# Performance work log

Hardware: AMD Instinct MI355X
Metric: run time of the kernel (lower is better)

The kernel has to match this reference:

```python
import jax, jax.numpy as jnp
import numpy as np

B, S, IN, OUT, RANK, NLANG = 4, 4096, 1024, 4096, 32, 9


def setup_inputs() -> dict:
    key = jax.random.key(0)
    k_x, k_w, k_w1 = jax.random.split(key, 3)
    x = jax.random.normal(k_x, (B, S, IN), dtype=jnp.float32)
    # base Linear weight (xavier-uniform in torch; gaussian fine for a numeric baseline)
    weight = jax.random.normal(k_w, (OUT, IN), dtype=jnp.float32) * 0.02
    bias = jnp.zeros((OUT,), dtype=jnp.float32)
    # per-language low-rank factors; torch inits w1 ~ N(0, 0.01), w2 zeros --
    # use small random values for both so gradients/outputs are non-trivial
    w1 = jax.random.normal(k_w1, (NLANG, OUT, RANK), dtype=jnp.float32) * 0.01
    w2 = jax.random.normal(jax.random.fold_in(key, 7), (NLANG, RANK, IN), dtype=jnp.float32) * 0.01
    return {"x": x, "weight": weight, "bias": bias, "w1": w1, "w2": w2,
            "src_id": 0, "tgt_id": 3}


def reference(x, weight, bias, w1, w2, src_id, tgt_id):
    # pair LMS delta: full [OUT, IN] low-rank matrix, as in the torch module
    delta = w1[src_id] @ w2[tgt_id]          # [OUT, RANK] @ [RANK, IN] -> [OUT, IN]
    w_eff = weight + delta
    # F.linear: x @ W^T + b
    return jnp.einsum('bsi,oi->bso', x, w_eff) + bias
```

## Files before the change

kernel.cpp:

```cpp
#include <hip/hip_runtime.h>

#define B_DIM 4
#define S_DIM 4096
#define IN_DIM 1024
#define OUT_DIM 4096
#define RANK_DIM 32

#define M_DIM (B_DIM * S_DIM)
#define N_DIM OUT_DIM
#define K_DIM IN_DIM

#define CVT_BLOCKS ((M_DIM * K_DIM) / 1024)

typedef _Float16 h4 __attribute__((ext_vector_type(4)));
typedef _Float16 h8 __attribute__((ext_vector_type(8)));
typedef float f32x16 __attribute__((ext_vector_type(16)));

__device__ __forceinline__ void async_load16(const void* g, void* l) {
  __builtin_amdgcn_global_load_lds((const __attribute__((address_space(1))) void*)g,
                                   (__attribute__((address_space(3))) void*)l,
                                   16, 0, 0);
}

__global__ __launch_bounds__(256) void prep_fused_kernel(
    const float4* __restrict__ x, h4* __restrict__ xh,
    const float* __restrict__ weight, const float* __restrict__ w1,
    const float* __restrict__ w2, const int* __restrict__ src_id,
    const int* __restrict__ tgt_id, h4* __restrict__ weff) {
  if (blockIdx.x < CVT_BLOCKS) {
    const int i = blockIdx.x * 256 + threadIdx.x;
    const float4 v = x[i];
    h4 o;
    o[0] = (_Float16)v.x; o[1] = (_Float16)v.y;
    o[2] = (_Float16)v.z; o[3] = (_Float16)v.w;
    xh[i] = o;
  } else {
    const int n = blockIdx.x - CVT_BLOCKS;
    const int src = src_id[0];
    const int tgt = tgt_id[0];
    __shared__ float w1r[RANK_DIM];
    if (threadIdx.x < RANK_DIM)
      w1r[threadIdx.x] = w1[((size_t)src * OUT_DIM + n) * RANK_DIM + threadIdx.x];
    __syncthreads();
    const int k4 = threadIdx.x;
    float4 acc = ((const float4*)(weight + (size_t)n * IN_DIM))[k4];
    const float* w2t = w2 + (size_t)tgt * RANK_DIM * IN_DIM;
#pragma unroll 8
    for (int r = 0; r < RANK_DIM; ++r) {
      const float4 wv = ((const float4*)(w2t + (size_t)r * IN_DIM))[k4];
      const float c = w1r[r];
      acc.x += c * wv.x; acc.y += c * wv.y; acc.z += c * wv.z; acc.w += c * wv.w;
    }
    h4 o;
    o[0] = (_Float16)acc.x; o[1] = (_Float16)acc.y;
    o[2] = (_Float16)acc.z; o[3] = (_Float16)acc.w;
    weff[(size_t)n * (IN_DIM / 4) + k4] = o;
  }
}

__global__ __launch_bounds__(256) void lms_gemm_kernel(
    const _Float16* __restrict__ A,
    const _Float16* __restrict__ Bt,
    const float* __restrict__ bias,
    float* __restrict__ C) {
  __shared__ _Float16 sA[128 * 64];
  __shared__ _Float16 sB[128 * 64];
  const int tid = threadIdx.x;
  const int wave = tid >> 6;
  const int lane = tid & 63;
  const int bn = blockIdx.x;
  const int bm = blockIdx.y;
  const int wm = wave & 1;
  const int wn = wave >> 1;

  f32x16 acc[2][2] = {};

  const int srow = lane >> 3;
  const int scol = ((lane & 7) ^ srow) * 8;
  const _Float16* gA = A + ((size_t)(bm * 128 + wave * 32 + srow)) * K_DIM + scol;
  const _Float16* gB = Bt + ((size_t)(bn * 128 + wave * 32 + srow)) * K_DIM + scol;
  _Float16* lA = &sA[(wave * 32) * 64];
  _Float16* lB = &sB[(wave * 32) * 64];

  for (int k0 = 0; k0 < K_DIM; k0 += 64) {
#pragma unroll
    for (int i = 0; i < 4; ++i) {
      async_load16(gA + (size_t)i * 8 * K_DIM + k0, lA + i * 8 * 64);
      async_load16(gB + (size_t)i * 8 * K_DIM + k0, lB + i * 8 * 64);
    }
    __syncthreads();

#pragma unroll
    for (int ks = 0; ks < 4; ++ks) {
      const int kq = ks * 2 + (lane >> 5);
      const int cs = (kq ^ (lane & 7)) * 8;
      h8 af[2], bf[2];
#pragma unroll
      for (int mi = 0; mi < 2; ++mi)
        af[mi] = *(const h8*)&sA[(wm * 64 + mi * 32 + (lane & 31)) * 64 + cs];
#pragma unroll
      for (int ni = 0; ni < 2; ++ni)
        bf[ni] = *(const h8*)&sB[(wn * 64 + ni * 32 + (lane & 31)) * 64 + cs];
#pragma unroll
      for (int mi = 0; mi < 2; ++mi)
#pragma unroll
        for (int ni = 0; ni < 2; ++ni)
          acc[mi][ni] = __builtin_amdgcn_mfma_f32_32x32x16_f16(af[mi], bf[ni],
                                                               acc[mi][ni], 0, 0, 0);
    }
    __syncthreads();
  }

  const int cn = lane & 31;
  const int rq = (lane >> 5) * 4;
#pragma unroll
  for (int ni = 0; ni < 2; ++ni) {
    const int col = bn * 128 + wn * 64 + ni * 32 + cn;
    const float bv = bias[col];
#pragma unroll
    for (int mi = 0; mi < 2; ++mi) {
      const int rowb = bm * 128 + wm * 64 + mi * 32 + rq;
      float* cp = C + (size_t)rowb * N_DIM + col;
#pragma unroll
      for (int reg = 0; reg < 16; ++reg) {
        const int roff = (reg & 3) + 8 * (reg >> 2);
        cp[(size_t)roff * N_DIM] = acc[mi][ni][reg] + bv;
      }
    }
  }
}

extern "C" void kernel_launch(void* const* d_in, const int* in_sizes, int n_in,
                              void* d_out, int out_size, void* d_ws, size_t ws_size,
                              hipStream_t stream) {
  const float* x      = (const float*)d_in[0];
  const float* weight = (const float*)d_in[1];
  const float* bias   = (const float*)d_in[2];
  const float* w1     = (const float*)d_in[3];
  const float* w2     = (const float*)d_in[4];
  const int* src_id   = (const int*)d_in[5];
  const int* tgt_id   = (const int*)d_in[6];
  float* out          = (float*)d_out;

  _Float16* xh   = (_Float16*)d_ws;
  _Float16* weff = xh + (size_t)M_DIM * K_DIM;

  prep_fused_kernel<<<CVT_BLOCKS + N_DIM, 256, 0, stream>>>(
      (const float4*)x, (h4*)xh, weight, w1, w2, src_id, tgt_id, (h4*)weff);

  dim3 grid(N_DIM / 128, M_DIM / 128);
  lms_gemm_kernel<<<grid, 256, 0, stream>>>(xh, weff, bias, out);
}
```

Measured before the change: 470.0 us.

## Rewrite GEMM as 256x256 double-buffered 8-wave kernel with prefetch and priority hints

Replaces the 128x128 single-buffered GEMM with a 256x256 tile using 512 threads, double-buffered LDS, and async prefetch of the next K tile issued while the current one is computed. It interleaves LDS fragment reads with MFMA phases under s_setprio and s_barrier, and remaps block IDs so neighbouring blocks share tiles in cache. The aim is to raise data reuse per load and hide global-load latency behind MFMA work. In exchange it uses 128KB of LDS per block and more registers, which limits occupancy.

Measured after the change: 497.7 us. 1.06x slower.

```diff
diff --git a/kernel.cpp b/kernel.cpp
--- a/kernel.cpp
+++ b/kernel.cpp
@@ -58,73 +58,120 @@
   }
 }
 
-__global__ __launch_bounds__(256) void lms_gemm_kernel(
+__device__ __forceinline__ void ktile_body(
+    const _Float16* cA, const _Float16* cB,
+    _Float16* nA, _Float16* nB,
+    const _Float16* gA0, const _Float16* gB0,
+    int kNext, bool doStage, int wave,
+    int aBase, int bBase, int kq, int key,
+    f32x16 (&acc)[4][2]) {
+  h8 b0[4], b1[4], a[4];
+#pragma unroll
+  for (int ks = 0; ks < 4; ++ks) {
+    const int co = (((ks * 2 + kq) ^ key) << 3);
+    b0[ks] = *(const h8*)&cB[bBase + co];
+    b1[ks] = *(const h8*)&cB[bBase + 2048 + co];
+    a[ks]  = *(const h8*)&cA[aBase + co];
+  }
+  if (doStage) {
+#pragma unroll
+    for (int i = 0; i < 4; ++i) {
+      async_load16(gA0 + (size_t)i * 64 * K_DIM + kNext, nA + i * 4096 + wave * 512);
+      async_load16(gB0 + (size_t)i * 64 * K_DIM + kNext, nB + i * 4096 + wave * 512);
+    }
+  }
+  __builtin_amdgcn_s_barrier();
+  __builtin_amdgcn_s_setprio(1);
+#pragma unroll
+  for (int ks = 0; ks < 4; ++ks) {
+    acc[0][0] = __builtin_amdgcn_mfma_f32_32x32x16_f16(a[ks], b0[ks], acc[0][0], 0, 0, 0);
+    acc[0][1] = __builtin_amdgcn_mfma_f32_32x32x16_f16(a[ks], b1[ks], acc[0][1], 0, 0, 0);
+  }
+  __builtin_amdgcn_s_setprio(0);
+  __builtin_amdgcn_s_barrier();
+#pragma unroll
+  for (int p = 1; p < 4; ++p) {
+    h8 ap[4];
+#pragma unroll
+    for (int ks = 0; ks < 4; ++ks)
+      ap[ks] = *(const h8*)&cA[aBase + p * 2048 + (((ks * 2 + kq) ^ key) << 3)];
+    __builtin_amdgcn_s_barrier();
+    __builtin_amdgcn_s_setprio(1);
+#pragma unroll
+    for (int ks = 0; ks < 4; ++ks) {
+      acc[p][0] = __builtin_amdgcn_mfma_f32_32x32x16_f16(ap[ks], b0[ks], acc[p][0], 0, 0, 0);
+      acc[p][1] = __builtin_amdgcn_mfma_f32_32x32x16_f16(ap[ks], b1[ks], acc[p][1], 0, 0, 0);
+    }
+    __builtin_amdgcn_s_setprio(0);
+    if (p < 3) __builtin_amdgcn_s_barrier();
+  }
+  asm volatile("s_waitcnt vmcnt(0)" ::: "memory");
+  __builtin_amdgcn_s_barrier();
+}
+
+__global__ __launch_bounds__(512, 2) void lms_gemm256_kernel(
     const _Float16* __restrict__ A,
     const _Float16* __restrict__ Bt,
     const float* __restrict__ bias,
     float* __restrict__ C) {
-  __shared__ _Float16 sA[128 * 64];
-  __shared__ _Float16 sB[128 * 64];
+  __shared__ _Float16 sA0[256 * 64];
+  __shared__ _Float16 sA1[256 * 64];
+  __shared__ _Float16 sB0[256 * 64];
+  __shared__ _Float16 sB1[256 * 64];
+
   const int tid = threadIdx.x;
   const int wave = tid >> 6;
   const int lane = tid & 63;
-  const int bn = blockIdx.x;
-  const int bm = blockIdx.y;
-  const int wm = wave & 1;
-  const int wn = wave >> 1;
 
-  f32x16 acc[2][2] = {};
+  const int bid = blockIdx.x;
+  const int wg = (bid & 7) * 128 + (bid >> 3);
+  const int bm = wg >> 4;
+  const int bn = wg & 15;
 
-  const int srow = lane >> 3;
-  const int scol = ((lane & 7) ^ srow) * 8;
-  const _Float16* gA = A + ((size_t)(bm * 128 + wave * 32 + srow)) * K_DIM + scol;
-  const _Float16* gB = Bt + ((size_t)(bn * 128 + wave * 32 + srow)) * K_DIM + scol;
-  _Float16* lA = &sA[(wave * 32) * 64];
-  _Float16* lB = &sB[(wave * 32) * 64];
+  const int wr = wave >> 2;
+  const int wc = wave & 3;
+  const int fr = lane & 31;
+  const int kq = lane >> 5;
+  const int key = fr & 7;
+  const int aBase = (wr * 128 + fr) * 64;
+  const int bBase = (wc * 64 + fr) * 64;
 
-  for (int k0 = 0; k0 < K_DIM; k0 += 64) {
-#pragma unroll
-    for (int i = 0; i < 4; ++i) {
-      async_load16(gA + (size_t)i * 8 * K_DIM + k0, lA + i * 8 * 64);
-      async_load16(gB + (size_t)i * 8 * K_DIM + k0, lB + i * 8 * 64);
-    }
-    __syncthreads();
+  const int srow = tid >> 3;
+  const int sblk = (tid & 7) ^ (srow & 7);
+  const _Float16* gA0 = A  + (size_t)(bm * 256 + srow) * K_DIM + sblk * 8;
+  const _Float16* gB0 = Bt + (size_t)(bn * 256 + srow) * K_DIM + sblk * 8;
+
+  f32x16 acc[4][2] = {};
 
 #pragma unroll
-    for (int ks = 0; ks < 4; ++ks) {
-      const int kq = ks * 2 + (lane >> 5);
-      const int cs = (kq ^ (lane & 7)) * 8;
-      h8 af[2], bf[2];
-#pragma unroll
-      for (int mi = 0; mi < 2; ++mi)
-        af[mi] = *(const h8*)&sA[(wm * 64 + mi * 32 + (lane & 31)) * 64 + cs];
-#pragma unroll
-      for (int ni = 0; ni < 2; ++ni)
-        bf[ni] = *(const h8*)&sB[(wn * 64 + ni * 32 + (lane & 31)) * 64 + cs];
-#pragma unroll
-      for (int mi = 0; mi < 2; ++mi)
-#pragma unroll
-        for (int ni = 0; ni < 2; ++ni)
-          acc[mi][ni] = __builtin_amdgcn_mfma_f32_32x32x16_f16(af[mi], bf[ni],
-                                                               acc[mi][ni], 0, 0, 0);
-    }
-    __syncthreads();
+  for (int i = 0; i < 4; ++i) {
+    async_load16(gA0 + (size_t)i * 64 * K_DIM, sA0 + i * 4096 + wave * 512);
+    async_load16(gB0 + (size_t)i * 64 * K_DIM, sB0 + i * 4096 + wave * 512);
+  }
+  asm volatile("s_waitcnt vmcnt(0)" ::: "memory");
+  __builtin_amdgcn_s_barrier();
+
+  for (int tt = 0; tt < 16; tt += 2) {
+    ktile_body(sA0, sB0, sA1, sB1, gA0, gB0, (tt + 1) * 64, true,
+               wave, aBase, bBase, kq, key, acc);
+    ktile_body(sA1, sB1, sA0, sB0, gA0, gB0, (tt + 2) * 64, (tt + 2) < 16,
+               wave, aBase, bBase, kq, key, acc);
   }
 
-  const int cn = lane & 31;
+  const int cn = fr;
   const int rq = (lane >> 5) * 4;
 #pragma unroll
   for (int ni = 0; ni < 2; ++ni) {
-    const int col = bn * 128 + wn * 64 + ni * 32 + cn;
+    const int col = bn * 256 + wc * 64 + ni * 32 + cn;
     const float bv = bias[col];
 #pragma unroll
-    for (int mi = 0; mi < 2; ++mi) {
-      const int rowb = bm * 128 + wm * 64 + mi * 32 + rq;
+    for (int p = 0; p < 4; ++p) {
+      const int rowb = bm * 256 + wr * 128 + p * 32 + rq;
       float* cp = C + (size_t)rowb * N_DIM + col;
 #pragma unroll
       for (int reg = 0; reg < 16; ++reg) {
         const int roff = (reg & 3) + 8 * (reg >> 2);
-        cp[(size_t)roff * N_DIM] = acc[mi][ni][reg] + bv;
+        cp[(size_t)roff * N_DIM] = acc[p][ni][reg] + bv;
       }
     }
   }
@@ -148,6 +195,5 @@
   prep_fused_kernel<<<CVT_BLOCKS + N_DIM, 256, 0, stream>>>(
       (const float4*)x, (h4*)xh, weight, w1, w2, src_id, tgt_id, (h4*)weff);
 
-  dim3 grid(N_DIM / 128, M_DIM / 128);
-  lms_gemm_kernel<<<grid, 256, 0, stream>>>(xh, weff, bias, out);
+  lms_gemm256_kernel<<<dim3(1024), dim3(512), 0, stream>>>(xh, weff, bias, out);
 }
```

## Rewrite GEMM as 256x256-tile, 4-stage async-pipelined kernel with XCD-aware block mapping

Applied to the files above, without the earlier changes.

Replaces the 128x128 single-buffered GEMM with a 256x256 tile computed by 512 threads, each wave holding a 4x2 grid of 32x32 MFMA accumulators. A 4-deep ring of LDS buffers (BK=32) is filled with global_load_lds, and explicit vmcnt waits plus barriers let loads for future stages overlap the current MFMAs instead of stalling on a barrier every step. Blocks are remapped across the 8 XCDs for L2 locality, and s_setprio raises priority around the MFMA bursts. The cost is more registers and 64KB of LDS per block, which limits occupancy, and hand-counted waitcnt values that must match the number of loads in flight.

Result: slower. 485.4 us (+3.3%).

```diff
diff --git a/kernel.cpp b/kernel.cpp
--- a/kernel.cpp
+++ b/kernel.cpp
@@ -58,68 +58,100 @@
   }
 }
 
-__global__ __launch_bounds__(256) void lms_gemm_kernel(
+__global__ __launch_bounds__(512, 2) void lms_gemm256_kernel(
     const _Float16* __restrict__ A,
     const _Float16* __restrict__ Bt,
     const float* __restrict__ bias,
     float* __restrict__ C) {
-  __shared__ _Float16 sA[128 * 64];
-  __shared__ _Float16 sB[128 * 64];
+  __shared__ _Float16 sA[4][8192];
+  __shared__ _Float16 sB[4][8192];
+
   const int tid = threadIdx.x;
   const int wave = tid >> 6;
   const int lane = tid & 63;
-  const int bn = blockIdx.x;
-  const int bm = blockIdx.y;
-  const int wm = wave & 1;
-  const int wn = wave >> 1;
 
-  f32x16 acc[2][2] = {};
+  const int bid = blockIdx.x;
+  const int wg = (bid & 7) * 128 + (bid >> 3);
+  const int bm = wg >> 4;
+  const int bn = wg & 15;
 
-  const int srow = lane >> 3;
-  const int scol = ((lane & 7) ^ srow) * 8;
-  const _Float16* gA = A + ((size_t)(bm * 128 + wave * 32 + srow)) * K_DIM + scol;
-  const _Float16* gB = Bt + ((size_t)(bn * 128 + wave * 32 + srow)) * K_DIM + scol;
-  _Float16* lA = &sA[(wave * 32) * 64];
-  _Float16* lB = &sB[(wave * 32) * 64];
+  const int wr = wave >> 2;
+  const int wc = wave & 3;
+  const int fr = lane & 31;
+  const int kq = lane >> 5;
+  const int key = (fr >> 1) & 3;
+  const int aBase = (wr * 128 + fr) * 32;
+  const int bBase = (wc * 64 + fr) * 32;
+  const int bo0 = (kq ^ key) << 3;
+  const int bo1 = bo0 ^ 16;
 
-  for (int k0 = 0; k0 < K_DIM; k0 += 64) {
-#pragma unroll
-    for (int i = 0; i < 4; ++i) {
-      async_load16(gA + (size_t)i * 8 * K_DIM + k0, lA + i * 8 * 64);
-      async_load16(gB + (size_t)i * 8 * K_DIM + k0, lB + i * 8 * 64);
-    }
-    __syncthreads();
+  const int srow = wave * 16 + (lane >> 2);
+  const int sblk = (lane & 3) ^ ((lane >> 3) & 3);
+  const _Float16* gA = A + (size_t)(bm * 256 + srow) * K_DIM + sblk * 8;
+  const _Float16* gB = Bt + (size_t)(bn * 256 + srow) * K_DIM + sblk * 8;
 
-#pragma unroll
-    for (int ks = 0; ks < 4; ++ks) {
-      const int kq = ks * 2 + (lane >> 5);
-      const int cs = (kq ^ (lane & 7)) * 8;
-      h8 af[2], bf[2];
-#pragma unroll
-      for (int mi = 0; mi < 2; ++mi)
-        af[mi] = *(const h8*)&sA[(wm * 64 + mi * 32 + (lane & 31)) * 64 + cs];
-#pragma unroll
-      for (int ni = 0; ni < 2; ++ni)
-        bf[ni] = *(const h8*)&sB[(wn * 64 + ni * 32 + (lane & 31)) * 64 + cs];
-#pragma unroll
-      for (int mi = 0; mi < 2; ++mi)
-#pragma unroll
-        for (int ni = 0; ni < 2; ++ni)
-          acc[mi][ni] = __builtin_amdgcn_mfma_f32_32x32x16_f16(af[mi], bf[ni],
-                                                               acc[mi][ni], 0, 0, 0);
-    }
-    __syncthreads();
+  f32x16 acc[4][2] = {};
+
+#define STAGE_TILE(nA, nB, KOFF)                                              \
+  {                                                                           \
+    async_load16(gA + (KOFF), (nA) + wave * 512);                             \
+    async_load16(gA + (KOFF) + 128 * K_DIM, (nA) + 4096 + wave * 512);        \
+    async_load16(gB + (KOFF), (nB) + wave * 512);                             \
+    async_load16(gB + (KOFF) + 128 * K_DIM, (nB) + 4096 + wave * 512);        \
   }
 
-  const int cn = lane & 31;
+#define KBODY(cA, cB, nA, nB, DO_STAGE, KOFF, WAITBAR)                        \
+  {                                                                           \
+    if (DO_STAGE) STAGE_TILE(nA, nB, KOFF);                                   \
+    h8 af[4][2], bf[2][2];                                                    \
+    _Pragma("unroll") for (int mi = 0; mi < 4; ++mi) {                        \
+      af[mi][0] = *(const h8*)&(cA)[aBase + mi * 1024 + bo0];                 \
+      af[mi][1] = *(const h8*)&(cA)[aBase + mi * 1024 + bo1];                 \
+    }                                                                         \
+    _Pragma("unroll") for (int ni = 0; ni < 2; ++ni) {                        \
+      bf[ni][0] = *(const h8*)&(cB)[bBase + ni * 1024 + bo0];                 \
+      bf[ni][1] = *(const h8*)&(cB)[bBase + ni * 1024 + bo1];                 \
+    }                                                                         \
+    __builtin_amdgcn_s_setprio(1);                                            \
+    _Pragma("unroll") for (int ks = 0; ks < 2; ++ks)                          \
+      _Pragma("unroll") for (int mi = 0; mi < 4; ++mi)                        \
+        _Pragma("unroll") for (int ni = 0; ni < 2; ++ni)                      \
+          acc[mi][ni] = __builtin_amdgcn_mfma_f32_32x32x16_f16(               \
+              af[mi][ks], bf[ni][ks], acc[mi][ni], 0, 0, 0);                  \
+    __builtin_amdgcn_s_setprio(0);                                            \
+    WAITBAR;                                                                  \
+  }
+
+#define WB8 asm volatile("s_waitcnt vmcnt(8) lgkmcnt(0)\ns_barrier" ::: "memory")
+#define WB4 asm volatile("s_waitcnt vmcnt(4) lgkmcnt(0)\ns_barrier" ::: "memory")
+#define WB0 asm volatile("s_waitcnt vmcnt(0) lgkmcnt(0)\ns_barrier" ::: "memory")
+
+  STAGE_TILE(sA[0], sB[0], 0);
+  STAGE_TILE(sA[1], sB[1], 32);
+  STAGE_TILE(sA[2], sB[2], 64);
+  asm volatile("s_waitcnt vmcnt(8)\ns_barrier" ::: "memory");
+
+  for (int t = 0; t < 28; t += 4) {
+    const int ko = t * 32;
+    KBODY(sA[0], sB[0], sA[3], sB[3], true, ko + 96,  WB8);
+    KBODY(sA[1], sB[1], sA[0], sB[0], true, ko + 128, WB8);
+    KBODY(sA[2], sB[2], sA[1], sB[1], true, ko + 160, WB8);
+    KBODY(sA[3], sB[3], sA[2], sB[2], true, ko + 192, WB8);
+  }
+  KBODY(sA[0], sB[0], sA[3], sB[3], true, 31 * 32, WB8);
+  KBODY(sA[1], sB[1], sA[0], sB[0], false, 0, WB4);
+  KBODY(sA[2], sB[2], sA[1], sB[1], false, 0, WB0);
+  KBODY(sA[3], sB[3], sA[2], sB[2], false, 0, (void)0);
+
+  const int cn = fr;
   const int rq = (lane >> 5) * 4;
 #pragma unroll
   for (int ni = 0; ni < 2; ++ni) {
-    const int col = bn * 128 + wn * 64 + ni * 32 + cn;
+    const int col = bn * 256 + wc * 64 + ni * 32 + cn;
     const float bv = bias[col];
 #pragma unroll
-    for (int mi = 0; mi < 2; ++mi) {
-      const int rowb = bm * 128 + wm * 64 + mi * 32 + rq;
+    for (int mi = 0; mi < 4; ++mi) {
+      const int rowb = bm * 256 + wr * 128 + mi * 32 + rq;
       float* cp = C + (size_t)rowb * N_DIM + col;
 #pragma unroll
       for (int reg = 0; reg < 16; ++reg) {
@@ -148,6 +180,5 @@
   prep_fused_kernel<<<CVT_BLOCKS + N_DIM, 256, 0, stream>>>(
       (const float4*)x, (h4*)xh, weight, w1, w2, src_id, tgt_id, (h4*)weff);
 
-  dim3 grid(N_DIM / 128, M_DIM / 128);
-  lms_gemm_kernel<<<grid, 256, 0, stream>>>(xh, weff, bias, out);
+  lms_gemm256_kernel<<<dim3(1024), dim3(512), 0, stream>>>(xh, weff, bias, out);
 }
```

## Double-buffer LDS tiles in GEMM to overlap async loads with MFMA

Applied to the files above, without the earlier changes.

Turns the GEMM main loop into a two-stage LDS ping-pong, where the next K tile's global-to-LDS async loads are issued before computing on the current buffer. It also preloads all fragments for the tile before the MFMA burst and raises wave priority around the MFMAs. Explicit waitcnt plus barrier replaces the paired __syncthreads, and launch_bounds now requests two blocks per CU. The aim is to hide global load latency behind compute, at the cost of twice the LDS (64 KB per block) and more registers for the fragments.

After: 491.7 us. 4.6% more time.

```diff
diff --git a/kernel.cpp b/kernel.cpp
--- a/kernel.cpp
+++ b/kernel.cpp
@@ -58,13 +58,13 @@
   }
 }
 
-__global__ __launch_bounds__(256) void lms_gemm_kernel(
+__global__ __launch_bounds__(256, 2) void lms_gemm_kernel(
     const _Float16* __restrict__ A,
     const _Float16* __restrict__ Bt,
     const float* __restrict__ bias,
     float* __restrict__ C) {
-  __shared__ _Float16 sA[128 * 64];
-  __shared__ _Float16 sB[128 * 64];
+  __shared__ _Float16 sA[2][128 * 64];
+  __shared__ _Float16 sB[2][128 * 64];
   const int tid = threadIdx.x;
   const int wave = tid >> 6;
   const int lane = tid & 63;
@@ -79,37 +79,52 @@
   const int scol = ((lane & 7) ^ srow) * 8;
   const _Float16* gA = A + ((size_t)(bm * 128 + wave * 32 + srow)) * K_DIM + scol;
   const _Float16* gB = Bt + ((size_t)(bn * 128 + wave * 32 + srow)) * K_DIM + scol;
-  _Float16* lA = &sA[(wave * 32) * 64];
-  _Float16* lB = &sB[(wave * 32) * 64];
 
-  for (int k0 = 0; k0 < K_DIM; k0 += 64) {
-#pragma unroll
-    for (int i = 0; i < 4; ++i) {
-      async_load16(gA + (size_t)i * 8 * K_DIM + k0, lA + i * 8 * 64);
-      async_load16(gB + (size_t)i * 8 * K_DIM + k0, lB + i * 8 * 64);
-    }
-    __syncthreads();
+#define STAGE(BUF, KOFF)                                                      \
+  {                                                                           \
+    _Pragma("unroll") for (int i = 0; i < 4; ++i) {                           \
+      async_load16(gA + (size_t)i * 8 * K_DIM + (KOFF),                       \
+                   &sA[BUF][(wave * 32 + i * 8) * 64]);                       \
+      async_load16(gB + (size_t)i * 8 * K_DIM + (KOFF),                       \
+                   &sB[BUF][(wave * 32 + i * 8) * 64]);                       \
+    }                                                                         \
+  }
 
-#pragma unroll
-    for (int ks = 0; ks < 4; ++ks) {
-      const int kq = ks * 2 + (lane >> 5);
-      const int cs = (kq ^ (lane & 7)) * 8;
-      h8 af[2], bf[2];
-#pragma unroll
-      for (int mi = 0; mi < 2; ++mi)
-        af[mi] = *(const h8*)&sA[(wm * 64 + mi * 32 + (lane & 31)) * 64 + cs];
-#pragma unroll
-      for (int ni = 0; ni < 2; ++ni)
-        bf[ni] = *(const h8*)&sB[(wn * 64 + ni * 32 + (lane & 31)) * 64 + cs];
-#pragma unroll
-      for (int mi = 0; mi < 2; ++mi)
-#pragma unroll
-        for (int ni = 0; ni < 2; ++ni)
-          acc[mi][ni] = __builtin_amdgcn_mfma_f32_32x32x16_f16(af[mi], bf[ni],
-                                                               acc[mi][ni], 0, 0, 0);
-    }
-    __syncthreads();
+#define KBODY(CUR, NXT, KOFF, DO_STAGE, DO_WAIT)                              \
+  {                                                                           \
+    if (DO_STAGE) STAGE(NXT, KOFF);                                           \
+    h8 af[4][2], bf[4][2];                                                    \
+    _Pragma("unroll") for (int ks = 0; ks < 4; ++ks) {                        \
+      const int kq = ks * 2 + (lane >> 5);                                    \
+      const int cs = (kq ^ (lane & 7)) * 8;                                   \
+      _Pragma("unroll") for (int mi = 0; mi < 2; ++mi)                        \
+        af[ks][mi] =                                                          \
+            *(const h8*)&sA[CUR][(wm * 64 + mi * 32 + (lane & 31)) * 64 + cs];\
+      _Pragma("unroll") for (int ni = 0; ni < 2; ++ni)                        \
+        bf[ks][ni] =                                                          \
+            *(const h8*)&sB[CUR][(wn * 64 + ni * 32 + (lane & 31)) * 64 + cs];\
+    }                                                                         \
+    __builtin_amdgcn_s_setprio(1);                                            \
+    _Pragma("unroll") for (int ks = 0; ks < 4; ++ks)                          \
+      _Pragma("unroll") for (int mi = 0; mi < 2; ++mi)                        \
+        _Pragma("unroll") for (int ni = 0; ni < 2; ++ni)                      \
+          acc[mi][ni] = __builtin_amdgcn_mfma_f32_32x32x16_f16(               \
+              af[ks][mi], bf[ks][ni], acc[mi][ni], 0, 0, 0);                  \
+    __builtin_amdgcn_s_setprio(0);                                            \
+    if (DO_WAIT)                                                              \
+      asm volatile("s_waitcnt vmcnt(0) lgkmcnt(0)\ns_barrier" ::: "memory");  \
   }
+
+  STAGE(0, 0);
+  asm volatile("s_waitcnt vmcnt(0)\ns_barrier" ::: "memory");
+
+#pragma unroll 1
+  for (int t = 0; t < 14; t += 2) {
+    KBODY(0, 1, (t + 1) * 64, true, true);
+    KBODY(1, 0, (t + 2) * 64, true, true);
+  }
+  KBODY(0, 1, 15 * 64, true, true);
+  KBODY(1, 0, 0, false, false);
 
   const int cn = lane & 31;
   const int rq = (lane >> 5) * 4;
```
